# Kernel optimization log

Measured on AMD Instinct MI355X. Metric: run time of the kernel, lower is better.

## Reference

```python
import math
import jax, jax.numpy as jnp
import numpy as np

B, H_IN, W_IN = 8, 16, 16
K, STRIDE = 3, 2
IN_CAPS, OUT_CAPS = 32, 32
P_SIZE, P_DIM = 16, 4
NUM_ROUTING = 3
EPS = 1e-8
LAMBDA_0, LAMBDA_DELTA = 0.001, 0.0001
LN_2PI = math.log(2.0 * math.pi)
C_IN = IN_CAPS * (P_SIZE + 1)  # 544


def setup_inputs() -> dict:
    key = jax.random.key(0)
    k1, k2 = jax.random.split(key)
    x = jax.random.uniform(k1, (B, H_IN, W_IN, C_IN), dtype=jnp.float32)
    # weights: [K*K*in_caps, out_caps, p_dim, p_dim] (leading 1 dim of torch param dropped)
    weights = jax.random.normal(k2, (K * K * IN_CAPS, OUT_CAPS, P_DIM, P_DIM), dtype=jnp.float32)
    beta_u = jnp.full((OUT_CAPS,), 0.1, dtype=jnp.float32)
    beta_a = jnp.full((OUT_CAPS,), 0.1, dtype=jnp.float32)
    return {"input_tensor": x, "weights": weights, "beta_u": beta_u, "beta_a": beta_a}


def _kernel_tile(x):
    # x: [B, H, W, C] -> [B, K, K, oh, ow, C]
    in_h, in_w = x.shape[1:3]
    end = in_w - K + 1
    tf = np.array([[s + k for s in range(0, end, STRIDE)] for k in range(K)])  # [K, out]
    out = x[:, tf]            # [B, K, oh, W, C]
    out = out[:, :, :, tf]    # [B, K, oh, K, ow, C]
    out = jnp.transpose(out, (0, 1, 3, 2, 4, 5))  # [B, K, K, oh, ow, C]
    oh = (in_h - K + 1) // STRIDE
    ow = (in_w - K + 1) // STRIDE
    return out, oh, ow


def _matrix_transform(poses, weights):
    # poses: [N, KKL, 16] -> votes: [N, KKL, out_caps, 16]
    n = poses.shape[0]
    p4 = poses.reshape(n, -1, P_DIM, P_DIM)
    votes = jnp.einsum('nkij,kojm->nkoim', p4, weights)
    return votes.reshape(n, -1, OUT_CAPS, P_SIZE)


def _m_step(act_in, r, votes, lam, beta_u, beta_a):
    r = r * act_in                                     # [N, KKL, out]
    r = r / (r.sum(axis=2, keepdims=True) + EPS)
    r_sum = r.sum(axis=1, keepdims=True)               # [N, 1, out]
    r_prob = (r / (r_sum + EPS))[..., None]            # [N, KKL, out, 1]
    mean = (r_prob * votes).sum(axis=1, keepdims=True)  # [N, 1, out, 16]
    std = jnp.sqrt((r_prob * (votes - mean) ** 2).sum(axis=1, keepdims=True) + EPS)
    r_sum_v = r_sum.reshape(-1, OUT_CAPS, 1)
    std_v = std.reshape(-1, OUT_CAPS, P_SIZE)
    cost = (beta_u[:, None] + jnp.log(std_v)) * r_sum_v
    act_out = jax.nn.sigmoid(lam * (beta_a - cost.sum(axis=-1)))  # [N, out]
    return act_out, mean, std_v[:, None]               # std: [N, 1, out, 16]


def _e_step(mean, std, act_out, votes):
    ln_p = -(votes - mean) ** 2 / (2.0 * std ** 2) - jnp.log(std) - LN_2PI / 2.0
    ln_ap = ln_p.sum(axis=3) + jnp.log(act_out.reshape(-1, 1, OUT_CAPS))
    return jax.nn.softmax(ln_ap, axis=-1)


def _em_routing(votes, act_in, beta_u, beta_a):
    n = votes.shape[0]
    r = jnp.full(votes.shape[:-1], 1.0 / OUT_CAPS, dtype=votes.dtype)
    lam = LAMBDA_0
    mean = act_out = None
    for t in range(NUM_ROUTING):
        lam += LAMBDA_DELTA
        act_out, mean, std = _m_step(act_in, r, votes, lam, beta_u, beta_a)
        if t < NUM_ROUTING - 1:
            r = _e_step(mean, std, act_out, votes)
    return mean, act_out


def reference(input_tensor, weights, beta_u, beta_a):
    bsz = input_tensor.shape[0]
    tiled, oh, ow = _kernel_tile(input_tensor)               # [B,K,K,oh,ow,544]
    # faithful row-major reshapes (match torch .contiguous().view)
    poses = tiled[..., :-IN_CAPS].reshape(-1, K * K * IN_CAPS, P_SIZE)
    acts = tiled[..., -IN_CAPS:].reshape(-1, K * K * IN_CAPS, 1)
    votes = _matrix_transform(poses, weights)                # [N, KKL, out, 16]
    mean, act_out = _em_routing(votes, acts, beta_u, beta_a)
    poses_out = mean.reshape(bsz, oh, ow, OUT_CAPS * P_SIZE)
    act_out = act_out.reshape(bsz, oh, ow, OUT_CAPS)
    return jnp.concatenate([poses_out, act_out], axis=-1)    # [B, oh, ow, 544]
```

## Files before the change

kernel.cpp:

```cpp
#include <hip/hip_runtime.h>


namespace {

constexpr int NKK = 288;
constexpr float EPSF = 1e-8f;
constexpr float LN2PI = 1.8378770664093453f;

typedef float f32x2 __attribute__((ext_vector_type(2)));

__device__ __forceinline__ float fastrcp(float x) { return __builtin_amdgcn_rcpf(x); }
__device__ __forceinline__ f32x2 splat2(float x) { f32x2 r; r.x = x; r.y = x; return r; }
__device__ __forceinline__ f32x2 fma2(f32x2 a, f32x2 b, f32x2 c) {
    return __builtin_elementwise_fma(a, b, c);
}

template <int CTRL>
__device__ __forceinline__ float dppf(float x) {
    return __int_as_float(__builtin_amdgcn_update_dpp(
        __float_as_int(x), __float_as_int(x), CTRL, 0xF, 0xF, false));
}
__device__ __forceinline__ float swz16(float x) {
    return __int_as_float(__builtin_amdgcn_ds_swizzle(__float_as_int(x), 0x401F));
}

__device__ __forceinline__ float redmax32(float v) {
    v = fmaxf(v, dppf<0xB1>(v));
    v = fmaxf(v, dppf<0x4E>(v));
    v = fmaxf(v, dppf<0x141>(v));
    v = fmaxf(v, dppf<0x140>(v));
    v = fmaxf(v, swz16(v));
    return v;
}
__device__ __forceinline__ float redsum32(float v) {
    v += dppf<0xB1>(v);
    v += dppf<0x4E>(v);
    v += dppf<0x141>(v);
    v += dppf<0x140>(v);
    v += swz16(v);
    return v;
}

__global__ __launch_bounds__(512, 4)
void caps_em_kernel(const float* __restrict__ x,
                    const float* __restrict__ Wg,
                    const float* __restrict__ bu,
                    const float* __restrict__ ba,
                    float* __restrict__ out)
{
    __shared__ float p4[NKK * 16];
    __shared__ float cIn[NKK];
    __shared__ float scr[8 * 32 * 33];
    __shared__ float meanS[32 * 17];
    __shared__ float i2vS[32 * 17];
    __shared__ float actS[32];
    __shared__ float baseS[32];

    const int n = blockIdx.x;
    const int t = threadIdx.x;

    for (int idx = t; idx < NKK * 16; idx += 512) {
        unsigned g = (unsigned)n * 4608u + (unsigned)idx;
        unsigned c = g & 511u, rest = g >> 9;
        unsigned ow = rest % 7u; rest /= 7u;
        unsigned oh = rest % 7u; rest /= 7u;
        unsigned kw = rest % 3u; rest /= 3u;
        unsigned kh = rest % 3u;
        unsigned b  = rest / 3u;
        p4[idx] = x[((b*16u + 2u*oh + kh)*16u + 2u*ow + kw)*544u + c];
    }
    for (int idx = t; idx < NKK; idx += 512) {
        unsigned g = (unsigned)n * 288u + (unsigned)idx;
        unsigned c = g & 31u, rest = g >> 5;
        unsigned ow = rest % 7u; rest /= 7u;
        unsigned oh = rest % 7u; rest /= 7u;
        unsigned kw = rest % 3u; rest /= 3u;
        unsigned kh = rest % 3u;
        unsigned b  = rest / 3u;
        const float a = x[((b*16u + 2u*oh + kh)*16u + 2u*ow + kw)*544u + 512u + c];
        cIn[idx] = a / (a + EPSF);
    }
    __syncthreads();

    const int o  = t & 31;
    const int kc = t >> 5;
    const int oo = t >> 4;
    const int pp = t & 15;

    float lam = 1.0e-3f;

    for (int it = 0; it < 3; ++it) {
        lam += 1.0e-4f;

        float S0 = 0.f;
        f32x2 Svp[8], Sv2p[8];
        #pragma unroll
        for (int q = 0; q < 8; ++q) { Svp[q] = splat2(0.f); Sv2p[q] = splat2(0.f); }

        if (it == 0) {
            #pragma unroll 2
            for (int kk = 0; kk < 18; ++kk) {
                const int k = kc*18 + kk;
                const float w = cIn[k] * 0.03125f;
                const f32x2 w2 = splat2(w);
                float P[16]; f32x2 Wl2[8];
                #pragma unroll
                for (int j = 0; j < 4; ++j) {
                    const float4 v4 = *(const float4*)&p4[k*16 + 4*j];
                    P[4*j] = v4.x; P[4*j+1] = v4.y; P[4*j+2] = v4.z; P[4*j+3] = v4.w;
                    const float4 w4 = *(const float4*)&Wg[(k*32 + o)*16 + 4*j];
                    f32x2 lo; lo.x = w4.x; lo.y = w4.y;
                    f32x2 hi; hi.x = w4.z; hi.y = w4.w;
                    Wl2[2*j] = lo; Wl2[2*j+1] = hi;
                }
                S0 += w;
                #pragma unroll
                for (int i = 0; i < 4; ++i) {
                    #pragma unroll
                    for (int h = 0; h < 2; ++h) {
                        const int q = i*2 + h;
                        f32x2 acc = splat2(P[i*4]) * Wl2[h];
                        acc = fma2(splat2(P[i*4+1]), Wl2[2+h], acc);
                        acc = fma2(splat2(P[i*4+2]), Wl2[4+h], acc);
                        acc = fma2(splat2(P[i*4+3]), Wl2[6+h], acc);
                        const f32x2 wv = w2 * acc;
                        Svp[q] += wv;
                        Sv2p[q] = fma2(wv, acc, Sv2p[q]);
                    }
                }
            }
        } else {
            f32x2 M2[8], I2[8];
            #pragma unroll
            for (int q = 0; q < 8; ++q) {
                f32x2 m; m.x = meanS[o*17 + 2*q]; m.y = meanS[o*17 + 2*q + 1];
                f32x2 iv; iv.x = i2vS[o*17 + 2*q]; iv.y = i2vS[o*17 + 2*q + 1];
                M2[q] = m; I2[q] = iv;
            }
            const float base = baseS[o];
            for (int kk = 0; kk < 18; ++kk) {
                const int k = kc*18 + kk;
                float P[16]; f32x2 Wl2[8];
                #pragma unroll
                for (int j = 0; j < 4; ++j) {
                    const float4 v4 = *(const float4*)&p4[k*16 + 4*j];
                    P[4*j] = v4.x; P[4*j+1] = v4.y; P[4*j+2] = v4.z; P[4*j+3] = v4.w;
                    const float4 w4 = *(const float4*)&Wg[(k*32 + o)*16 + 4*j];
                    f32x2 lo; lo.x = w4.x; lo.y = w4.y;
                    f32x2 hi; hi.x = w4.z; hi.y = w4.w;
                    Wl2[2*j] = lo; Wl2[2*j+1] = hi;
                }
                f32x2 v2[8];
                f32x2 sa[4];
                #pragma unroll
                for (int i = 0; i < 4; ++i) {
                    sa[i] = splat2(0.f);
                    #pragma unroll
                    for (int h = 0; h < 2; ++h) {
                        const int q = i*2 + h;
                        f32x2 acc = splat2(P[i*4]) * Wl2[h];
                        acc = fma2(splat2(P[i*4+1]), Wl2[2+h], acc);
                        acc = fma2(splat2(P[i*4+2]), Wl2[4+h], acc);
                        acc = fma2(splat2(P[i*4+3]), Wl2[6+h], acc);
                        v2[q] = acc;
                        const f32x2 d = acc - M2[q];
                        sa[i] = fma2(d * d, I2[q], sa[i]);
                    }
                }
                const f32x2 sv = (sa[0] + sa[1]) + (sa[2] + sa[3]);
                const float lnp = base - (sv.x + sv.y);
                const float mx = redmax32(lnp);
                const float e  = __expf(lnp - mx);
                const float ss = redsum32(e);
                const float u = e * fastrcp(ss) * cIn[k];
                S0 += u;
                const f32x2 u2 = splat2(u);
                #pragma unroll
                for (int q = 0; q < 8; ++q) {
                    const f32x2 uv = u2 * v2[q];
                    Svp[q] += uv;
                    Sv2p[q] = fma2(uv, v2[q], Sv2p[q]);
                }
            }
        }

        S0 += __shfl_xor(S0, 32, 64);
        #pragma unroll
        for (int q = 0; q < 8; ++q) {
            f32x2 ta, tb;
            ta.x = __shfl_xor(Svp[q].x, 32, 64);
            ta.y = __shfl_xor(Svp[q].y, 32, 64);
            tb.x = __shfl_xor(Sv2p[q].x, 32, 64);
            tb.y = __shfl_xor(Sv2p[q].y, 32, 64);
            Svp[q] += ta;
            Sv2p[q] += tb;
        }
        if ((kc & 1) == 0) {
            float* row = &scr[((kc >> 1)*32 + o)*33];
            #pragma unroll
            for (int q = 0; q < 8; ++q) {
                row[2*q]      = Svp[q].x;  row[2*q + 1]      = Svp[q].y;
                row[16 + 2*q] = Sv2p[q].x; row[16 + 2*q + 1] = Sv2p[q].y;
            }
            row[32] = S0;
        }
        __syncthreads();

        {
            float sm = 0.f, s2 = 0.f, rs = 0.f;
            #pragma unroll
            for (int q = 0; q < 8; ++q) {
                const int b0 = (q*32 + oo)*33;
                sm += scr[b0 + pp];
                s2 += scr[b0 + 16 + pp];
                rs += scr[b0 + 32];
            }
            const float inv = 1.0f / (rs + EPSF);
            const float S1  = rs * inv;
            const float m   = sm * inv;
            float var = s2 * inv - m*m*(2.0f - S1);
            var = fmaxf(var, 0.0f) + EPSF;
            meanS[oo*17 + pp] = m;
            i2vS [oo*17 + pp] = 0.5f / var;
            scr[oo*33 + pp] = 0.5f * __logf(var);
        }
        __syncthreads();
        if (t < 32) {
            float lsum = 0.f;
            #pragma unroll
            for (int p = 0; p < 16; ++p) lsum += scr[t*33 + p];
            float rs = 0.f;
            #pragma unroll
            for (int q = 0; q < 8; ++q) rs += scr[(q*32 + t)*33 + 32];
            const float cost = (16.0f * bu[t] + lsum) * rs;
            const float ao   = 1.0f / (1.0f + __expf(-lam * (ba[t] - cost)));
            actS[t]  = ao;
            baseS[t] = -lsum - 8.0f*LN2PI + __logf(ao);
        }
        __syncthreads();
    }

    for (int idx = t; idx < 544; idx += 512) {
        const float v = (idx < 512) ? meanS[(idx >> 4)*17 + (idx & 15)]
                                    : actS[idx - 512];
        out[n*544 + idx] = v;
    }
}

}

extern "C" void kernel_launch(void* const* d_in, const int* in_sizes, int n_in,
                              void* d_out, int out_size, void* d_ws, size_t ws_size,
                              hipStream_t stream) {
    (void)in_sizes; (void)n_in; (void)out_size; (void)d_ws; (void)ws_size;
    const float* x  = (const float*)d_in[0];
    const float* W  = (const float*)d_in[1];
    const float* bu = (const float*)d_in[2];
    const float* ba = (const float*)d_in[3];
    float* out = (float*)d_out;
    caps_em_kernel<<<dim3(392), dim3(512), 0, stream>>>(x, W, bu, ba, out);
}
```

Measured before the change: 126.0 us.

## Double-buffer weight loads and hoist softmax max out of E-step loop

Restructures both routing loops so the next capsule's weight block (Wg) is fetched into a second register buffer while the current votes are computed, hiding global-load latency. In the E-step, the per-iteration max reduction is replaced by a single max over the base terms computed once before the loop. Since lnp is always at most base, this still gives a valid upper bound for the softmax stabilisation. That bound is looser, though, so exp can underflow if the squared-distance terms are large. The change also adds register pressure from the second weight buffer and forces unroll 1.

```diff
diff --git a/kernel.cpp b/kernel.cpp
--- a/kernel.cpp
+++ b/kernel.cpp
@@ -14,6 +14,8 @@
 __device__ __forceinline__ f32x2 fma2(f32x2 a, f32x2 b, f32x2 c) {
     return __builtin_elementwise_fma(a, b, c);
 }
+__device__ __forceinline__ f32x2 lo2(float4 v) { f32x2 r; r.x = v.x; r.y = v.y; return r; }
+__device__ __forceinline__ f32x2 hi2(float4 v) { f32x2 r; r.x = v.z; r.y = v.w; return r; }
 
 template <int CTRL>
 __device__ __forceinline__ float dppf(float x) {
@@ -89,6 +91,89 @@
 
     float lam = 1.0e-3f;
 
+#define LOAD_P(K_)                                                         \
+    float P[16];                                                           \
+    {                                                                      \
+        const float4 p0 = *(const float4*)&p4[(K_)*16 + 0];                \
+        const float4 p1 = *(const float4*)&p4[(K_)*16 + 4];                \
+        const float4 p2 = *(const float4*)&p4[(K_)*16 + 8];                \
+        const float4 p3 = *(const float4*)&p4[(K_)*16 + 12];               \
+        P[0]=p0.x; P[1]=p0.y; P[2]=p0.z; P[3]=p0.w;                        \
+        P[4]=p1.x; P[5]=p1.y; P[6]=p1.z; P[7]=p1.w;                        \
+        P[8]=p2.x; P[9]=p2.y; P[10]=p2.z; P[11]=p2.w;                      \
+        P[12]=p3.x; P[13]=p3.y; P[14]=p3.z; P[15]=p3.w;                    \
+    }
+
+#define LOAD_W(WD, K_)                                                     \
+    {                                                                      \
+        const float4* wp_ = (const float4*)&Wg[((K_)*32 + o)*16];          \
+        WD[0] = wp_[0]; WD[1] = wp_[1]; WD[2] = wp_[2]; WD[3] = wp_[3];    \
+    }
+
+#define VOTES(WCUR, V2)                                                    \
+    _Pragma("unroll")                                                      \
+    for (int i = 0; i < 4; ++i) {                                          \
+        _Pragma("unroll")                                                  \
+        for (int h = 0; h < 2; ++h) {                                      \
+            const f32x2 w0 = (h == 0) ? lo2(WCUR[0]) : hi2(WCUR[0]);       \
+            const f32x2 w1 = (h == 0) ? lo2(WCUR[1]) : hi2(WCUR[1]);       \
+            const f32x2 w2 = (h == 0) ? lo2(WCUR[2]) : hi2(WCUR[2]);       \
+            const f32x2 w3 = (h == 0) ? lo2(WCUR[3]) : hi2(WCUR[3]);       \
+            f32x2 acc = splat2(P[i*4]) * w0;                               \
+            acc = fma2(splat2(P[i*4+1]), w1, acc);                         \
+            acc = fma2(splat2(P[i*4+2]), w2, acc);                         \
+            acc = fma2(splat2(P[i*4+3]), w3, acc);                         \
+            V2[i*2 + h] = acc;                                             \
+        }                                                                  \
+    }
+
+#define M0_BODY(K_, WCUR, KN_, WNXT)                                       \
+    {                                                                      \
+        const int k_ = (K_);                                               \
+        LOAD_P(k_)                                                         \
+        f32x2 v2[8];                                                       \
+        VOTES(WCUR, v2)                                                    \
+        LOAD_W(WNXT, (KN_))                                                \
+        const float w_ = cIn[k_] * 0.03125f;                               \
+        const f32x2 w2_ = splat2(w_);                                      \
+        S0 += w_;                                                          \
+        _Pragma("unroll")                                                  \
+        for (int q = 0; q < 8; ++q) {                                      \
+            const f32x2 wv = w2_ * v2[q];                                  \
+            Svp[q] += wv;                                                  \
+            Sv2p[q] = fma2(wv, v2[q], Sv2p[q]);                            \
+        }                                                                  \
+    }
+
+#define E_BODY(K_, WCUR, KN_, WNXT)                                        \
+    {                                                                      \
+        const int k_ = (K_);                                               \
+        LOAD_P(k_)                                                         \
+        f32x2 v2[8];                                                       \
+        VOTES(WCUR, v2)                                                    \
+        LOAD_W(WNXT, (KN_))                                                \
+        f32x2 saA = splat2(0.f), saB = splat2(0.f);                        \
+        _Pragma("unroll")                                                  \
+        for (int q = 0; q < 8; ++q) {                                      \
+            const f32x2 d = v2[q] - M2[q];                                 \
+            if (q & 1) saB = fma2(d * d, I2[q], saB);                      \
+            else       saA = fma2(d * d, I2[q], saA);                      \
+        }                                                                  \
+        const f32x2 sab = saA + saB;                                       \
+        const float lnp = base - (sab.x + sab.y);                          \
+        const float e  = __expf(lnp - Mb);                                 \
+        const float ss = redsum32(e);                                      \
+        const float u = e * fastrcp(ss) * cIn[k_];                         \
+        S0 += u;                                                           \
+        const f32x2 u2 = splat2(u);                                        \
+        _Pragma("unroll")                                                  \
+        for (int q = 0; q < 8; ++q) {                                      \
+            const f32x2 uv = u2 * v2[q];                                   \
+            Svp[q] += uv;                                                  \
+            Sv2p[q] = fma2(uv, v2[q], Sv2p[q]);                            \
+        }                                                                  \
+    }
+
     for (int it = 0; it < 3; ++it) {
         lam += 1.0e-4f;
 
@@ -97,37 +182,17 @@
         #pragma unroll
         for (int q = 0; q < 8; ++q) { Svp[q] = splat2(0.f); Sv2p[q] = splat2(0.f); }
 
+        const int k0 = kc * 18;
+        float4 Wa[4], Wb[4];
+        LOAD_W(Wa, k0)
+
         if (it == 0) {
-            #pragma unroll 2
-            for (int kk = 0; kk < 18; ++kk) {
-                const int k = kc*18 + kk;
-                const float w = cIn[k] * 0.03125f;
-                const f32x2 w2 = splat2(w);
-                float P[16]; f32x2 Wl2[8];
-                #pragma unroll
-                for (int j = 0; j < 4; ++j) {
-                    const float4 v4 = *(const float4*)&p4[k*16 + 4*j];
-                    P[4*j] = v4.x; P[4*j+1] = v4.y; P[4*j+2] = v4.z; P[4*j+3] = v4.w;
-                    const float4 w4 = *(const float4*)&Wg[(k*32 + o)*16 + 4*j];
-                    f32x2 lo; lo.x = w4.x; lo.y = w4.y;
-                    f32x2 hi; hi.x = w4.z; hi.y = w4.w;
-                    Wl2[2*j] = lo; Wl2[2*j+1] = hi;
-                }
-                S0 += w;
-                #pragma unroll
-                for (int i = 0; i < 4; ++i) {
-                    #pragma unroll
-                    for (int h = 0; h < 2; ++h) {
-                        const int q = i*2 + h;
-                        f32x2 acc = splat2(P[i*4]) * Wl2[h];
-                        acc = fma2(splat2(P[i*4+1]), Wl2[2+h], acc);
-                        acc = fma2(splat2(P[i*4+2]), Wl2[4+h], acc);
-                        acc = fma2(splat2(P[i*4+3]), Wl2[6+h], acc);
-                        const f32x2 wv = w2 * acc;
-                        Svp[q] += wv;
-                        Sv2p[q] = fma2(wv, acc, Sv2p[q]);
-                    }
-                }
+            #pragma unroll 1
+            for (int kk = 0; kk < 18; kk += 2) {
+                const int k = k0 + kk;
+                M0_BODY(k, Wa, k + 1, Wb)
+                int kn2 = k + 2; if (kn2 >= NKK) kn2 = 0;
+                M0_BODY(k + 1, Wb, kn2, Wa)
             }
         } else {
             f32x2 M2[8], I2[8];
@@ -138,49 +203,13 @@
                 M2[q] = m; I2[q] = iv;
             }
             const float base = baseS[o];
-            for (int kk = 0; kk < 18; ++kk) {
-                const int k = kc*18 + kk;
-                float P[16]; f32x2 Wl2[8];
-                #pragma unroll
-                for (int j = 0; j < 4; ++j) {
-                    const float4 v4 = *(const float4*)&p4[k*16 + 4*j];
-                    P[4*j] = v4.x; P[4*j+1] = v4.y; P[4*j+2] = v4.z; P[4*j+3] = v4.w;
-                    const float4 w4 = *(const float4*)&Wg[(k*32 + o)*16 + 4*j];
-                    f32x2 lo; lo.x = w4.x; lo.y = w4.y;
-                    f32x2 hi; hi.x = w4.z; hi.y = w4.w;
-                    Wl2[2*j] = lo; Wl2[2*j+1] = hi;
-                }
-                f32x2 v2[8];
-                f32x2 sa[4];
-                #pragma unroll
-                for (int i = 0; i < 4; ++i) {
-                    sa[i] = splat2(0.f);
-                    #pragma unroll
-                    for (int h = 0; h < 2; ++h) {
-                        const int q = i*2 + h;
-                        f32x2 acc = splat2(P[i*4]) * Wl2[h];
-                        acc = fma2(splat2(P[i*4+1]), Wl2[2+h], acc);
-                        acc = fma2(splat2(P[i*4+2]), Wl2[4+h], acc);
-                        acc = fma2(splat2(P[i*4+3]), Wl2[6+h], acc);
-                        v2[q] = acc;
-                        const f32x2 d = acc - M2[q];
-                        sa[i] = fma2(d * d, I2[q], sa[i]);
-                    }
-                }
-                const f32x2 sv = (sa[0] + sa[1]) + (sa[2] + sa[3]);
-                const float lnp = base - (sv.x + sv.y);
-                const float mx = redmax32(lnp);
-                const float e  = __expf(lnp - mx);
-                const float ss = redsum32(e);
-                const float u = e * fastrcp(ss) * cIn[k];
-                S0 += u;
-                const f32x2 u2 = splat2(u);
-                #pragma unroll
-                for (int q = 0; q < 8; ++q) {
-                    const f32x2 uv = u2 * v2[q];
-                    Svp[q] += uv;
-                    Sv2p[q] = fma2(uv, v2[q], Sv2p[q]);
-                }
+            const float Mb = redmax32(base);
+            #pragma unroll 1
+            for (int kk = 0; kk < 18; kk += 2) {
+                const int k = k0 + kk;
+                E_BODY(k, Wa, k + 1, Wb)
+                int kn2 = k + 2; if (kn2 >= NKK) kn2 = 0;
+                E_BODY(k + 1, Wb, kn2, Wa)
             }
         }
 
@@ -240,6 +269,12 @@
         __syncthreads();
     }
 
+#undef LOAD_P
+#undef LOAD_W
+#undef VOTES
+#undef M0_BODY
+#undef E_BODY
+
     for (int idx = t; idx < 544; idx += 512) {
         const float v = (idx < 512) ? meanS[(idx >> 4)*17 + (idx & 15)]
                                     : actS[idx - 512];
```

After: 140.4 us. 1.11x slower.
